# Kernel tuning notes

Measured on AMD Instinct MI355X. Metric: run time of the kernel, lower is better.

The kernel has to match this reference:

```python
import jax, jax.numpy as jnp
import numpy as np

ATTN_DIM = 1024
LATENT_DIM = 1024
N_HEADS = 16
HEAD_SIZE = ATTN_DIM // N_HEADS


def setup_inputs() -> dict:
    key = jax.random.key(0)
    ks = jax.random.split(key, 7)
    B, T = 2, 2048
    s_in = 1.0 / np.sqrt(LATENT_DIM)
    s_a = 1.0 / np.sqrt(ATTN_DIM)
    return {
        "x": jax.random.normal(ks[0], (B, T, LATENT_DIM), jnp.float32),
        "w_attn": jax.random.normal(ks[1], (LATENT_DIM, ATTN_DIM), jnp.float32) * s_in,
        "b_attn": jnp.zeros((ATTN_DIM,), jnp.float32),
        "w_qkv": jax.random.normal(ks[2], (ATTN_DIM, 3 * ATTN_DIM), jnp.float32) * s_a,
        "b_qkv": jnp.zeros((3 * ATTN_DIM,), jnp.float32),
        "w_proj": jax.random.normal(ks[3], (ATTN_DIM, ATTN_DIM), jnp.float32) * s_a,
        "b_proj": jnp.zeros((ATTN_DIM,), jnp.float32),
    }


def reference(x, w_attn, b_attn, w_qkv, b_qkv, w_proj, b_proj):
    # x: [B, T, latent_dim]
    h = jnp.einsum("btl,lc->btc", x, w_attn) + b_attn  # [B,T,C]
    B, T, C = h.shape
    qkv = jnp.einsum("btc,cd->btd", h, w_qkv) + b_qkv  # [B,T,3C]
    q, k, v = jnp.split(qkv, 3, axis=2)
    def heads(t):  # [B,T,C] -> [B,H,T,hs]
        return t.reshape(B, T, N_HEADS, HEAD_SIZE).transpose(0, 2, 1, 3)
    q, k, v = heads(q), heads(k), heads(v)
    scale = 1.0 / np.sqrt(HEAD_SIZE)
    scores = jnp.einsum("bhqd,bhkd->bhqk", q, k) * scale  # [B,H,T,T]
    attn = jax.nn.softmax(scores, axis=-1)
    out = jnp.einsum("bhqk,bhkd->bhqd", attn, v)  # [B,H,T,hs]
    out = out.transpose(0, 2, 1, 3).reshape(B, T, C)
    return jnp.einsum("btc,cd->btd", out, w_proj) + b_proj
```

## Files before the change

### kernel.cpp

```cpp
#include <hip/hip_runtime.h>

typedef unsigned short u16;
typedef unsigned int u32;
typedef __bf16 bf16x8 __attribute__((ext_vector_type(8)));
typedef float f32x4 __attribute__((ext_vector_type(4)));
typedef float f32x16 __attribute__((ext_vector_type(16)));
typedef unsigned uint2v __attribute__((ext_vector_type(2)));

typedef const __attribute__((address_space(1))) void* gcp_t;
typedef __attribute__((address_space(3))) void* lp_t;
#define GLDS16(g, l) __builtin_amdgcn_global_load_lds((gcp_t)(g), (lp_t)(l), 16, 0, 0)

__device__ __forceinline__ u16 f2bf(float f) {
  unsigned int u = __builtin_bit_cast(unsigned int, f);
  u += 0x7fffu + ((u >> 16) & 1u);
  return (u16)(u >> 16);
}
__device__ __forceinline__ u16 bfc(float f) {
  return __builtin_bit_cast(u16, (__bf16)f);
}
__device__ __forceinline__ u32 pkbf(float lo, float hi) {
  return (u32)bfc(lo) | ((u32)bfc(hi) << 16);
}
__device__ __forceinline__ float ex2(float x) {
  return __builtin_amdgcn_exp2f(x);
}

__global__ __launch_bounds__(256) void prep(const float* __restrict__ x, u16* __restrict__ xb,
                                            const float* __restrict__ wa, u16* __restrict__ wTa,
                                            const float* __restrict__ wq, u16* __restrict__ wTq,
                                            const float* __restrict__ wp, u16* __restrict__ wTp) {
  __shared__ float tile[32][33];
  const int idx = (int)blockIdx.x;
  const int tid = (int)threadIdx.x;
  if (idx < 2048) {
    long i = ((long)idx * 256 + tid) * 8;
    float4 a = *(const float4*)(x + i);
    float4 b = *(const float4*)(x + i + 4);
    union { u16 u[8]; int4 v; } pk;
    pk.u[0] = f2bf(a.x); pk.u[1] = f2bf(a.y); pk.u[2] = f2bf(a.z); pk.u[3] = f2bf(a.w);
    pk.u[4] = f2bf(b.x); pk.u[5] = f2bf(b.y); pk.u[6] = f2bf(b.z); pk.u[7] = f2bf(b.w);
    *(int4*)(xb + i) = pk.v;
    return;
  }
  const float* in; u16* out; int K, N, bx, by;
  if (idx < 3072) {
    int id = idx - 2048; in = wa; out = wTa; K = 1024; N = 1024; bx = id & 31; by = id >> 5;
  } else if (idx < 6144) {
    int id = idx - 3072; in = wq; out = wTq; K = 1024; N = 3072; bx = id % 96; by = id / 96;
  } else {
    int id = idx - 6144; in = wp; out = wTp; K = 1024; N = 1024; bx = id & 31; by = id >> 5;
  }
  const int n0 = bx * 32, k0 = by * 32;
  const int tx = tid & 31, ty = tid >> 5;
#pragma unroll
  for (int i = 0; i < 4; ++i)
    tile[ty + i * 8][tx] = in[(long)(k0 + ty + i * 8) * N + n0 + tx];
  __syncthreads();
#pragma unroll
  for (int i = 0; i < 4; ++i)
    out[(long)(n0 + ty + i * 8) * K + k0 + tx] = f2bf(tile[tx][ty + i * 8]);
}

template <int BM, int BN, int WN_WAVES, typename OutT, bool VSPLIT = false>
__global__ __launch_bounds__(256) void gemm_bt(const u16* __restrict__ A,
                                               const u16* __restrict__ Bt,
                                               const float* __restrict__ bias,
                                               OutT* __restrict__ C,
                                               u16* __restrict__ vout,
                                               int M, int N, int K) {
  constexpr int WM = BM / (4 / WN_WAVES);
  constexpr int WN = BN / WN_WAVES;
  constexpr int MF = WM / 16, NF = WN / 16;
  constexpr int STG = 2 * BM * 32 + 2 * BN * 32;
  constexpr int TRN = VSPLIT ? 128 * 136 : 0;
  constexpr int PSZ = STG > TRN ? STG : TRN;
  __shared__ __align__(16) u16 pool[PSZ];
  u16* lA0 = pool;
  u16* lB0 = pool + 2 * BM * 32;
  const int tid = (int)threadIdx.x;
  const int ln = tid & 63;
  const int w = tid >> 6;
  const int wr = w / WN_WAVES, wc = w % WN_WAVES;
  const int lr = ln & 15, lg = ln >> 4;
  const long mBase = (long)blockIdx.y * BM;
  const long nBase = (long)blockIdx.x * BN;

  f32x4 acc[MF][NF] = {};

  const int r0 = ln >> 2;
  const int c0 = (ln & 3) * 8;

  auto stage = [&](int buf, int k0) {
#pragma unroll
    for (int i = 0; i < BM / 64; ++i) {
      const int br = (i * 4 + w) * 16;
      GLDS16(A + (mBase + br + r0) * K + k0 + c0, lA0 + buf * BM * 32 + br * 32);
    }
#pragma unroll
    for (int i = 0; i < BN / 64; ++i) {
      const int br = (i * 4 + w) * 16;
      GLDS16(Bt + (nBase + br + r0) * K + k0 + c0, lB0 + buf * BN * 32 + br * 32);
    }
  };

  stage(0, 0);
  __syncthreads();
  int cur = 0;
  for (int k0 = 0; k0 < K; k0 += 32) {
    if (k0 + 32 < K) stage(cur ^ 1, k0 + 32);
    bf16x8 af[MF], bfv[NF];
#pragma unroll
    for (int mi = 0; mi < MF; ++mi)
      af[mi] = *(const bf16x8*)&lA0[cur * BM * 32 + (wr * WM + mi * 16 + lr) * 32 + lg * 8];
#pragma unroll
    for (int ni = 0; ni < NF; ++ni)
      bfv[ni] = *(const bf16x8*)&lB0[cur * BN * 32 + (wc * WN + ni * 16 + lr) * 32 + lg * 8];
#pragma unroll
    for (int mi = 0; mi < MF; ++mi)
#pragma unroll
      for (int ni = 0; ni < NF; ++ni)
        acc[mi][ni] = __builtin_amdgcn_mfma_f32_16x16x32_bf16(af[mi], bfv[ni],
                                                              acc[mi][ni], 0, 0, 0);
    __syncthreads();
    cur ^= 1;
  }

  if (VSPLIT && nBase >= 2048) {
#pragma unroll
    for (int ni = 0; ni < NF; ++ni) {
      const int cl = wc * WN + ni * 16 + lr;
      const float bv = bias[nBase + cl];
#pragma unroll
      for (int mi = 0; mi < MF; ++mi) {
#pragma unroll
        for (int j = 0; j < 4; ++j) {
          const int rl = wr * WM + mi * 16 + lg * 4 + j;
          pool[cl * 136 + rl] = bfc(acc[mi][ni][j] + bv);
        }
      }
    }
    __syncthreads();
    const int c = tid >> 1, half = tid & 1;
    const long cglob = nBase + c - 2048;
    const int hh2 = (int)(cglob >> 6), d = (int)(cglob & 63);
    const int bb = (int)(mBase >> 11);
    const int t0 = (int)(mBase & 2047);
    u16* dst = vout + ((long)(bb * 16 + hh2) * 64 + d) * 2048 + t0 + half * 64;
    const u16* srcp = &pool[c * 136 + half * 64];
#pragma unroll
    for (int i = 0; i < 8; ++i)
      *(int4*)(dst + i * 8) = *(const int4*)(srcp + i * 8);
    return;
  }

#pragma unroll
  for (int ni = 0; ni < NF; ++ni) {
    const long col = nBase + wc * WN + ni * 16 + lr;
    const float bv = bias[col];
#pragma unroll
    for (int mi = 0; mi < MF; ++mi) {
      const long row = mBase + wr * WM + mi * 16 + lg * 4;
#pragma unroll
      for (int j = 0; j < 4; ++j) {
        float v = acc[mi][ni][j] + bv;
        if constexpr (sizeof(OutT) == 2) {
          C[(row + j) * N + col] = (OutT)f2bf(v);
        } else {
          C[(row + j) * N + col] = v;
        }
      }
    }
  }
}

__global__ __launch_bounds__(512, 4) void attn_fwd(const u16* __restrict__ qkv,
                                                   const u16* __restrict__ vt,
                                                   u16* __restrict__ outp) {
  __shared__ __align__(16) u16 smemf[32768];
  const int tid = (int)threadIdx.x;
  const int ln = tid & 63;
  const int l31 = tid & 31;
  const int hiH = (tid >> 5) & 1;
  const int w = tid >> 6;
  const int g = w >> 2;
  const int qw = w & 3;
  const int bid = (int)blockIdx.x;
  const int qt = bid & 15;
  const int bh = bid >> 4;
  const int b = bh >> 4;
  const int hh = bh & 15;

  const float SCALE = 0.125f * 1.44269504088896f;

  const long qrow = (long)(b * 2048 + qt * 128 + qw * 32 + l31);
  const u16* Qp = qkv + qrow * 3072 + hh * 64;
  bf16x8 qf[4];
#pragma unroll
  for (int ks = 0; ks < 4; ++ks) {
    union { u16 u[8]; int4 i4; bf16x8 v; } in, ov;
    in.i4 = *(const int4*)(Qp + ks * 16 + hiH * 8);
#pragma unroll
    for (int e = 0; e < 8; ++e) {
      float f = __builtin_bit_cast(float, (u32)in.u[e] << 16) * SCALE;
      ov.u[e] = f2bf(f);
    }
    qf[ks] = ov.v;
  }
  bf16x8 onesv;
  {
    union { u16 u[8]; bf16x8 v; } o_;
#pragma unroll
    for (int e = 0; e < 8; ++e) o_.u[e] = 0x3F80;
    onesv = o_.v;
  }

  f32x16 o[2] = {};
  f32x16 lacc = {};
  float mrow = -1e30f;

  const u16* Kbase = qkv + ((long)b * 2048) * 3072 + 1024 + hh * 64;
  const u16* Vbase = vt + (long)bh * 64 * 2048;

  const int sr = ln >> 3;
  const int scm = ln & 7;

  const int sw = (l31 & 7) << 4;
  const char* lds0 = (const char*)smemf + g * 32768 + l31 * 128;
  const char* kbse[4];
#pragma unroll
  for (int ks = 0; ks < 4; ++ks) kbse[ks] = lds0 + ((ks * 32 + hiH * 16) ^ sw);

  auto stageKV = [&](int buf, int t) {
    const int kv0 = (g * 16 + t) * 64;
    u16* dstK = smemf + g * 16384 + buf * 8192;
#pragma unroll
    for (int i = 0; i < 2; ++i) {
      const int br = (i * 4 + qw) * 8;
      const int r = br + sr;
      const int cs = scm ^ (r & 7);
      GLDS16(Kbase + (long)(kv0 + r) * 3072 + cs * 8, dstK + br * 64);
      GLDS16(Vbase + (long)r * 2048 + kv0 + cs * 8, dstK + 4096 + br * 64);
    }
  };

  stageKV(0, 0);
  __syncthreads();

  auto tile = [&](int buf, int kt) {
    if (kt + 1 < 16) stageKV(buf ^ 1, kt + 1);
    const int boff = buf * 16384;

    f32x16 st[2] = {};
    __builtin_amdgcn_s_setprio(1);
#pragma unroll
    for (int t = 0; t < 2; ++t)
#pragma unroll
      for (int ks = 0; ks < 4; ++ks) {
        const bf16x8 kf = *(const bf16x8*)(kbse[ks] + boff + t * 4096);
        st[t] = __builtin_amdgcn_mfma_f32_32x32x16_bf16(kf, qf[ks], st[t], 0, 0, 0);
      }
    __builtin_amdgcn_s_setprio(0);

    float mv[32];
#pragma unroll
    for (int t = 0; t < 2; ++t)
#pragma unroll
      for (int r = 0; r < 16; ++r) mv[t * 16 + r] = st[t][r];
    float m1[11];
#pragma unroll
    for (int i = 0; i < 10; ++i)
      m1[i] = fmaxf(fmaxf(mv[3 * i], mv[3 * i + 1]), mv[3 * i + 2]);
    m1[10] = fmaxf(mv[30], mv[31]);
    float m2[4];
    m2[0] = fmaxf(fmaxf(m1[0], m1[1]), m1[2]);
    m2[1] = fmaxf(fmaxf(m1[3], m1[4]), m1[5]);
    m2[2] = fmaxf(fmaxf(m1[6], m1[7]), m1[8]);
    m2[3] = fmaxf(m1[9], m1[10]);
    float mx = fmaxf(fmaxf(fmaxf(m2[0], m2[1]), m2[2]), m2[3]);
    mx = fmaxf(mx, __shfl_xor(mx, 32));

    if (!__all(mx <= mrow + 8.0f)) {
      const float mnew = fmaxf(mrow, mx);
      const float sf = ex2(mrow - mnew);
      mrow = mnew;
      lacc[0] *= sf;
      o[0] *= sf;
      o[1] *= sf;
    }

#pragma unroll
    for (int t = 0; t < 2; ++t)
#pragma unroll
      for (int r = 0; r < 16; ++r) st[t][r] = ex2(st[t][r] - mrow);

    bf16x8 pa[4];
#pragma unroll
    for (int t = 0; t < 2; ++t)
#pragma unroll
      for (int gg = 0; gg < 2; ++gg) {
        const int bse = gg * 8;
        u32 A = pkbf(st[t][bse + 0], st[t][bse + 1]);
        u32 B = pkbf(st[t][bse + 2], st[t][bse + 3]);
        u32 C = pkbf(st[t][bse + 4], st[t][bse + 5]);
        u32 D = pkbf(st[t][bse + 6], st[t][bse + 7]);
        union { u32 wv[4]; bf16x8 v; } u;
#if __has_builtin(__builtin_amdgcn_permlane32_swap)
        uint2v r0 = __builtin_amdgcn_permlane32_swap(A, C, false, false);
        uint2v r1 = __builtin_amdgcn_permlane32_swap(B, D, false, false);
        u.wv[0] = r0[0]; u.wv[1] = r1[0]; u.wv[2] = r0[1]; u.wv[3] = r1[1];
#else
        const u32 sA = __shfl_xor((int)A, 32);
        const u32 sB = __shfl_xor((int)B, 32);
        const u32 sC = __shfl_xor((int)C, 32);
        const u32 sD = __shfl_xor((int)D, 32);
        u.wv[0] = hiH ? sC : A;
        u.wv[1] = hiH ? sD : B;
        u.wv[2] = hiH ? C : sA;
        u.wv[3] = hiH ? D : sB;
#endif
        pa[t * 2 + gg] = u.v;
      }

    __builtin_amdgcn_s_setprio(1);
#pragma unroll
    for (int ks2 = 0; ks2 < 4; ++ks2)
      lacc = __builtin_amdgcn_mfma_f32_32x32x16_bf16(onesv, pa[ks2], lacc, 0, 0, 0);
#pragma unroll
    for (int dt = 0; dt < 2; ++dt)
#pragma unroll
      for (int ks2 = 0; ks2 < 4; ++ks2) {
        const bf16x8 vf = *(const bf16x8*)(kbse[ks2] + boff + 8192 + dt * 4096);
        o[dt] = __builtin_amdgcn_mfma_f32_32x32x16_bf16(vf, pa[ks2], o[dt], 0, 0, 0);
      }
    __builtin_amdgcn_s_setprio(0);
    __syncthreads();
  };

  for (int k8 = 0; k8 < 8; ++k8) {
    tile(0, k8 * 2);
    tile(1, k8 * 2 + 1);
  }

  const float lsum_tot = lacc[0];
  float* PO = (float*)smemf;
  float* MLf = (float*)((char*)smemf + 32768);

  if (g == 1) {
    float* dst = PO + (w - 4) * 2048 + ln * 32;
#pragma unroll
    for (int dt = 0; dt < 2; ++dt)
#pragma unroll
      for (int q4 = 0; q4 < 4; ++q4) {
        f32x4 c;
#pragma unroll
        for (int j = 0; j < 4; ++j) c[j] = o[dt][q4 * 4 + j];
        *(f32x4*)(dst + dt * 16 + q4 * 4) = c;
      }
    MLf[(w - 4) * 128 + ln * 2] = mrow;
    MLf[(w - 4) * 128 + ln * 2 + 1] = lsum_tot;
  }
  __syncthreads();
  if (g == 0) {
    const float m1v = MLf[w * 128 + ln * 2];
    const float l1 = MLf[w * 128 + ln * 2 + 1];
    const float* src = PO + w * 2048 + ln * 32;
    const float m = fmaxf(mrow, m1v);
    const float a0 = ex2(mrow - m);
    const float a1 = ex2(m1v - m);
    const float linv = 1.0f / (lsum_tot * a0 + l1 * a1);
    u16* T = (u16*)((char*)smemf + 36864) + w * (32 * 72);
#pragma unroll
    for (int dt = 0; dt < 2; ++dt) {
      float o1[16];
#pragma unroll
      for (int q4 = 0; q4 < 4; ++q4) {
        const f32x4 c = *(const f32x4*)(src + dt * 16 + q4 * 4);
#pragma unroll
        for (int j = 0; j < 4; ++j) o1[q4 * 4 + j] = c[j];
      }
#pragma unroll
      for (int r = 0; r < 16; ++r) {
        const float v = (o[dt][r] * a0 + o1[r] * a1) * linv;
        const int d = (r & 3) + 8 * (r >> 2) + 4 * hiH + dt * 32;
        T[l31 * 72 + d] = bfc(v);
      }
    }
    asm volatile("s_waitcnt lgkmcnt(0)" ::: "memory");
    __builtin_amdgcn_sched_barrier(0);
    const int rr = ln >> 1;
    const int c0 = (ln & 1) * 32;
    u16* orow = outp + ((long)(b * 2048 + qt * 128 + w * 32 + rr)) * 1024 + hh * 64 + c0;
#pragma unroll
    for (int i = 0; i < 4; ++i)
      *(int4*)(orow + i * 8) = *(const int4*)&T[rr * 72 + c0 + i * 8];
  }
}

extern "C" void kernel_launch(void* const* d_in, const int* in_sizes, int n_in,
                              void* d_out, int out_size, void* d_ws, size_t ws_size,
                              hipStream_t stream) {
  (void)in_sizes; (void)n_in; (void)out_size;
  const float* x = (const float*)d_in[0];
  const float* b_attn = (const float*)d_in[2];
  const float* b_qkv = (const float*)d_in[4];
  const float* b_proj = (const float*)d_in[6];

  char* ws = (char*)d_ws;
  const size_t MB = 1024 * 1024;
  u16* xb   = (u16*)(ws + 0 * MB);
  u16* hbuf = (u16*)(ws + 8 * MB);
  u16* qkvb = (u16*)(ws + 16 * MB);
  u16* vtb  = (u16*)(ws + 40 * MB);
  u16* aout = (u16*)(ws + 48 * MB);
  u16* wTa  = (u16*)(ws + 56 * MB);
  u16* wTq  = (u16*)(ws + 58 * MB);
  u16* wTp  = (u16*)(ws + 64 * MB);
  if (ws_size < 66 * MB) return;

  prep<<<7168, 256, 0, stream>>>(x, xb, (const float*)d_in[1], wTa,
                                 (const float*)d_in[3], wTq,
                                 (const float*)d_in[5], wTp);

  gemm_bt<64, 128, 4, u16><<<dim3(8, 64), 256, 0, stream>>>(
      xb, wTa, b_attn, hbuf, nullptr, 4096, 1024, 1024);
  gemm_bt<128, 128, 2, u16, true><<<dim3(24, 32), 256, 0, stream>>>(
      hbuf, wTq, b_qkv, qkvb, vtb, 4096, 3072, 1024);
  attn_fwd<<<512, 512, 0, stream>>>(qkvb, vtb, aout);
  gemm_bt<64, 128, 4, float><<<dim3(8, 64), 256, 0, stream>>>(
      aout, wTp, b_proj, (float*)d_out, nullptr, 4096, 1024, 1024);
}
```

Before: 162.1 us.

## Swizzle block order for XCD locality and compute row sums with VALU

GEMM and attention blocks get remapped so that consecutive workgroups dispatched to the same XCD cover neighbouring tiles, which is meant to improve L2 reuse of shared operands. In attention, the softmax row sum is now taken with a VALU reduction over the fp32 probabilities plus a cross-half shuffle, replacing the extra MFMA against a ones vector. The s_setprio hints around the MFMA loops are removed. The row sum is now accumulated in fp32 instead of from bf16-rounded probabilities, and the swizzle relies on the grid size dividing by 8.

```diff
diff --git a/kernel.cpp b/kernel.cpp
--- a/kernel.cpp
+++ b/kernel.cpp
@@ -83,8 +83,15 @@
   const int w = tid >> 6;
   const int wr = w / WN_WAVES, wc = w % WN_WAVES;
   const int lr = ln & 15, lg = ln >> 4;
-  const long mBase = (long)blockIdx.y * BM;
-  const long nBase = (long)blockIdx.x * BN;
+
+  const int nwg = (int)(gridDim.x * gridDim.y);
+  const int lin = (int)(blockIdx.y * gridDim.x + blockIdx.x);
+  const int cpx = nwg >> 3;
+  const int swzb = (lin & 7) * cpx + (lin >> 3);
+  const int bx = swzb % (int)gridDim.x;
+  const int by = swzb / (int)gridDim.x;
+  const long mBase = (long)by * BM;
+  const long nBase = (long)bx * BN;
 
   f32x4 acc[MF][NF] = {};
 
@@ -185,7 +192,8 @@
   const int w = tid >> 6;
   const int g = w >> 2;
   const int qw = w & 3;
-  const int bid = (int)blockIdx.x;
+  const int bid0 = (int)blockIdx.x;
+  const int bid = ((bid0 & 7) << 6) | (bid0 >> 3);
   const int qt = bid & 15;
   const int bh = bid >> 4;
   const int b = bh >> 4;
@@ -207,17 +215,9 @@
     }
     qf[ks] = ov.v;
   }
-  bf16x8 onesv;
-  {
-    union { u16 u[8]; bf16x8 v; } o_;
-#pragma unroll
-    for (int e = 0; e < 8; ++e) o_.u[e] = 0x3F80;
-    onesv = o_.v;
-  }
 
   f32x16 o[2] = {};
-  f32x16 lacc = {};
-  float mrow = -1e30f;
+  float mrow = -1e30f, lsum = 0.f;
 
   const u16* Kbase = qkv + ((long)b * 2048) * 3072 + 1024 + hh * 64;
   const u16* Vbase = vt + (long)bh * 64 * 2048;
@@ -252,7 +252,6 @@
     const int boff = buf * 16384;
 
     f32x16 st[2] = {};
-    __builtin_amdgcn_s_setprio(1);
 #pragma unroll
     for (int t = 0; t < 2; ++t)
 #pragma unroll
@@ -260,7 +259,6 @@
         const bf16x8 kf = *(const bf16x8*)(kbse[ks] + boff + t * 4096);
         st[t] = __builtin_amdgcn_mfma_f32_32x32x16_bf16(kf, qf[ks], st[t], 0, 0, 0);
       }
-    __builtin_amdgcn_s_setprio(0);
 
     float mv[32];
 #pragma unroll
@@ -284,7 +282,7 @@
       const float mnew = fmaxf(mrow, mx);
       const float sf = ex2(mrow - mnew);
       mrow = mnew;
-      lacc[0] *= sf;
+      lsum *= sf;
       o[0] *= sf;
       o[1] *= sf;
     }
@@ -293,6 +291,16 @@
     for (int t = 0; t < 2; ++t)
 #pragma unroll
       for (int r = 0; r < 16; ++r) st[t][r] = ex2(st[t][r] - mrow);
+
+    float ts[16];
+#pragma unroll
+    for (int r = 0; r < 16; ++r) ts[r] = st[0][r] + st[1][r];
+#pragma unroll
+    for (int s = 8; s > 0; s >>= 1)
+#pragma unroll
+      for (int r = 0; r < 8; ++r)
+        if (r < s) ts[r] += ts[r + s];
+    lsum += ts[0];
 
     bf16x8 pa[4];
 #pragma unroll
@@ -322,10 +330,6 @@
         pa[t * 2 + gg] = u.v;
       }
 
-    __builtin_amdgcn_s_setprio(1);
-#pragma unroll
-    for (int ks2 = 0; ks2 < 4; ++ks2)
-      lacc = __builtin_amdgcn_mfma_f32_32x32x16_bf16(onesv, pa[ks2], lacc, 0, 0, 0);
 #pragma unroll
     for (int dt = 0; dt < 2; ++dt)
 #pragma unroll
@@ -333,7 +337,6 @@
         const bf16x8 vf = *(const bf16x8*)(kbse[ks2] + boff + 8192 + dt * 4096);
         o[dt] = __builtin_amdgcn_mfma_f32_32x32x16_bf16(vf, pa[ks2], o[dt], 0, 0, 0);
       }
-    __builtin_amdgcn_s_setprio(0);
     __syncthreads();
   };
 
@@ -342,7 +345,7 @@
     tile(1, k8 * 2 + 1);
   }
 
-  const float lsum_tot = lacc[0];
+  const float lsum_tot = lsum + __shfl_xor(lsum, 32);
   float* PO = (float*)smemf;
   float* MLf = (float*)((char*)smemf + 32768);
 
```

Result: faster. 151.3 us (-6.7%).
